# Kernel optimization log

Hardware: AMD Instinct MI355X
Metric: run time of the kernel (lower is better)

## Reference

```python
import jax, jax.numpy as jnp
import numpy as np

K = 1  # number of items to sample exactly
B, N = 512, 8192


def log1mexp(x):
    # log(1 - exp(x)) for x <= 0, numerically stable (Maechler 2012)
    return jnp.where(x > -jnp.log(2.0), jnp.log(-jnp.expm1(x)), jnp.log1p(-jnp.exp(x)))


def logaddexp_c(x1, x2):
    # custom logaddexp matching the torch module (handles -inf == -inf ties)
    delta = jnp.where(x1 == x2, 0.0, x1 - x2)
    return jnp.maximum(x1, x2) + jax.nn.softplus(-jnp.abs(delta))


def dp_table(logp, logq, kk):
    # a[b, i, c] = log Pr(exactly c-1 successes among first i items); shape [B, n+1, kk+2]
    bsz = logp.shape[0]
    state0 = jnp.full((bsz, kk + 2), -jnp.inf, logp.dtype).at[:, 1].set(0.0)
    ninf_col = jnp.full((bsz, 1), -jnp.inf, logp.dtype)

    def step(state, xs):
        lp, lq = xs  # each [B]
        grown = logaddexp_c(state[:, :-1] + lp[:, None], state[:, 1:] + lq[:, None])
        new = jnp.concatenate([ninf_col, grown], axis=1)
        return new, new

    _, rows = jax.lax.scan(step, state0, (logp.T, logq.T))  # rows: [n, B, kk+2]
    return jnp.concatenate([state0[None], rows], axis=0).transpose(1, 0, 2)


def sample_scan(a, logp, noise):
    # reverse DP sampling pass; a: [B, n+1, C], logp/noise: [B, n]
    bsz, np1, C = a.shape
    n = np1 - 1
    kcol = C - 1  # == K + 1 in table-column coordinates
    ap = a[:, :-1, :][:, ::-1].transpose(1, 0, 2)  # [n, B, C], row i-1 for i=n..1
    ac = a[:, 1:, :][:, ::-1].transpose(1, 0, 2)   # [n, B, C], row i   for i=n..1
    lp_rev = logp[:, ::-1].T                        # [n, B]
    u_rev = noise[:, ::-1].T                        # [n, B]

    def step(j, xs):
        ap_r, ac_r, lp_t, u_t = xs
        p = jnp.take_along_axis(ap_r, (j - 1)[:, None], axis=1)[:, 0]
        z = jnp.take_along_axis(ac_r, j[:, None], axis=1)[:, 0]
        p = jnp.minimum(p + lp_t - z, 0.0)  # conditional log-prob, clamp fp round-off
        q = log1mexp(p)
        X = (u_t < jax.nn.sigmoid(p - q)).astype(logp.dtype)  # Bernoulli(logits=p-q)
        j = jnp.where(X > 0, j - 1, j)
        return j, X

    j0 = jnp.full((bsz,), kcol, jnp.int32)
    _, Xs = jax.lax.scan(step, j0, (ap, ac, lp_rev, u_rev))  # Xs: [n, B]
    return Xs[::-1].T  # [B, n]


def setup_inputs() -> dict:
    key = jax.random.key(0)
    k1, k2 = jax.random.split(key)
    logits = jax.random.normal(k1, (B, N), dtype=jnp.float32)
    noise = jax.random.uniform(k2, (B, N), dtype=jnp.float32)
    return {"logits": logits, "noise": noise}


def reference(logits, noise):
    logp = jnp.minimum(jax.nn.log_sigmoid(logits), -1e-7)  # clamped log_sigmoid
    logq = log1mexp(logp)
    a = dp_table(logp, logq, K)       # [B, N+1, K+2]
    return sample_scan(a, logp, noise)  # [B, N] in {0,1}
```

## Files before the change

### kernel.cpp

```cpp
#include <hip/hip_runtime.h>
#include <math.h>

#define NB 512
#define NI 8192
#define NLOG2 0.69314718055994530942f

__device__ __forceinline__ float log1mexp_f(float x) {
    return (x > -NLOG2) ? logf(-expm1f(x)) : log1pf(-expf(x));
}

__global__ __launch_bounds__(256) void prep_kernel(const float* __restrict__ logits,
                                                   float* __restrict__ Alp,
                                                   float* __restrict__ Blq) {
    int idx = blockIdx.x * blockDim.x + threadIdx.x;
    float4 x4 = ((const float4*)logits)[idx];
    float4 lp4, lq4;
    const float* xs = &x4.x;
    float* lps = &lp4.x;
    float* lqs = &lq4.x;
#pragma unroll
    for (int j = 0; j < 4; ++j) {
        float x = xs[j];
        float lp = -(fmaxf(-x, 0.0f) + log1pf(expf(-fabsf(x))));
        lp = fminf(lp, -1e-7f);
        lps[j] = lp;
        lqs[j] = log1mexp_f(lp);
    }
    ((float4*)Alp)[idx] = lp4;
    ((float4*)Blq)[idx] = lq4;
}

#define CH 32
__device__ __forceinline__ void scan_step(float lp, float lq, float& S0, float& S1,
                                          float& x1o, float& s1o) {
    const float L2E = 1.44269504088896340736f;
    const float LN2 = 0.69314718055994530942f;
    float x1 = S0 + lp;
    float x2 = S1 + lq;
    float d  = x1 - x2;
    float m  = fmaxf(x1, x2);
    float z  = fabsf(d) * -L2E;
    float e  = __builtin_amdgcn_exp2f(z);
    float a  = 1.0f + e;
    float l  = __builtin_amdgcn_logf(a);
    S1 = fmaf(l, LN2, m);
    S0 = S0 + lq;
    x1o = x1;
    s1o = S1;
}

__global__ __launch_bounds__(64, 1) void scan_kernel(float* __restrict__ A,
                                                     float* __restrict__ B) {
    int row = blockIdx.x * blockDim.x + threadIdx.x;
    float* Ar = A + (size_t)row * NI;
    float* Br = B + (size_t)row * NI;

    float S0 = 0.0f;
    float S1 = -INFINITY;

    float lpA[CH], lqA[CH], lpB[CH], lqB[CH];
    float x1A[CH], s1A[CH], x1B[CH], s1B[CH];

#pragma unroll
    for (int j = 0; j < CH / 4; ++j) {
        *(float4*)&lpA[4 * j] = *(const float4*)&Ar[4 * j];
        *(float4*)&lqA[4 * j] = *(const float4*)&Br[4 * j];
    }

    const int NCHUNK = NI / CH;
    for (int c = 0; c < NCHUNK; c += 2) {
        const int base0 = c * CH, base1 = (c + 1) * CH, base2 = (c + 2) * CH;

#pragma unroll
        for (int j = 0; j < CH / 4; ++j) {
            *(float4*)&lpB[4 * j] = *(const float4*)&Ar[base1 + 4 * j];
            *(float4*)&lqB[4 * j] = *(const float4*)&Br[base1 + 4 * j];
        }

#pragma unroll
        for (int j = 0; j < CH; ++j)
            scan_step(lpA[j], lqA[j], S0, S1, x1A[j], s1A[j]);
#pragma unroll
        for (int j = 0; j < CH / 4; ++j) {
            *(float4*)&Ar[base0 + 4 * j] = *(float4*)&x1A[4 * j];
            *(float4*)&Br[base0 + 4 * j] = *(float4*)&s1A[4 * j];
        }

        if (c + 2 < NCHUNK) {
#pragma unroll
            for (int j = 0; j < CH / 4; ++j) {
                *(float4*)&lpA[4 * j] = *(const float4*)&Ar[base2 + 4 * j];
                *(float4*)&lqA[4 * j] = *(const float4*)&Br[base2 + 4 * j];
            }
        }

#pragma unroll
        for (int j = 0; j < CH; ++j)
            scan_step(lpB[j], lqB[j], S0, S1, x1B[j], s1B[j]);
#pragma unroll
        for (int j = 0; j < CH / 4; ++j) {
            *(float4*)&Ar[base1 + 4 * j] = *(float4*)&x1B[4 * j];
            *(float4*)&Br[base1 + 4 * j] = *(float4*)&s1B[4 * j];
        }
    }
}

__global__ __launch_bounds__(256) void decide_kernel(const float* __restrict__ A,
                                                     const float* __restrict__ S,
                                                     const float* __restrict__ noise,
                                                     float* __restrict__ out) {
    int row = blockIdx.x;
    const float4* x1r = (const float4*)(A + (size_t)row * NI);
    const float4* s1r = (const float4*)(S + (size_t)row * NI);
    const float4* ur = (const float4*)(noise + (size_t)row * NI);
    float4* outr = (float4*)(out + (size_t)row * NI);
    int tid = threadIdx.x;

    int best = -1;
#pragma unroll
    for (int k = 0; k < NI / 4 / 256; ++k) {
        int g = tid + k * 256;
        float4 x1 = x1r[g];
        float4 s1 = s1r[g];
        float4 u = ur[g];
#pragma unroll
        for (int j = 0; j < 4; ++j) {
            float p = fminf((&x1.x)[j] - (&s1.x)[j], 0.0f);
            float q = log1mexp_f(p);
            float z = p - q;
            float prob = 1.0f / (1.0f + expf(-z));
            if ((&u.x)[j] < prob) {
                int i = 4 * g + j;
                best = (i > best) ? i : best;
            }
        }
    }

#pragma unroll
    for (int off = 32; off > 0; off >>= 1) {
        int o = __shfl_down(best, off);
        best = (o > best) ? o : best;
    }
    __shared__ int lds[4];
    __shared__ int sel_s;
    int wid = tid >> 6;
    if ((tid & 63) == 0) lds[wid] = best;
    __syncthreads();
    if (tid == 0) {
        int s01 = (lds[0] > lds[1]) ? lds[0] : lds[1];
        int s23 = (lds[2] > lds[3]) ? lds[2] : lds[3];
        sel_s = (s01 > s23) ? s01 : s23;
    }
    __syncthreads();
    int sel = sel_s;

#pragma unroll
    for (int k = 0; k < NI / 4 / 256; ++k) {
        int g = tid + k * 256;
        int i0 = 4 * g;
        float4 v;
        v.x = (i0 == sel) ? 1.0f : 0.0f;
        v.y = (i0 + 1 == sel) ? 1.0f : 0.0f;
        v.z = (i0 + 2 == sel) ? 1.0f : 0.0f;
        v.w = (i0 + 3 == sel) ? 1.0f : 0.0f;
        outr[g] = v;
    }
}

extern "C" void kernel_launch(void* const* d_in, const int* in_sizes, int n_in,
                              void* d_out, int out_size, void* d_ws, size_t ws_size,
                              hipStream_t stream) {
    (void)in_sizes; (void)n_in; (void)out_size; (void)ws_size;
    const float* logits = (const float*)d_in[0];
    const float* noise = (const float*)d_in[1];
    float* out = (float*)d_out;
    float* A = (float*)d_ws;

    int total4 = NB * NI / 4;
    prep_kernel<<<total4 / 256, 256, 0, stream>>>(logits, A, out);
    scan_kernel<<<8, 64, 0, stream>>>(A, out);
    decide_kernel<<<NB, 256, 0, stream>>>(A, out, noise, out);
}
```

Before: 484.3 us.

## Fuse prep, DP scan and sampling decision into a single per-row kernel

Merges the three kernels into one. Each thread computes log-sigmoid and log1mexp inline with hardware exp2/log2 intrinsics, runs the forward recurrence, and applies the Bernoulli test on the fly while keeping the last accepted index. The one-hot output is then written per block. This removes the workspace round-trips (writing and re-reading the x1 and S1 arrays) and two kernel launches. In exchange it puts more ALU work on the serial critical path of only 8 blocks of 64 threads, uses fast approximate transcendentals that may differ slightly near decision thresholds, and simplifies sigmoid(p-q) to exp(p).

```diff
diff --git a/kernel.cpp b/kernel.cpp
--- a/kernel.cpp
+++ b/kernel.cpp
@@ -3,68 +3,57 @@
 
 #define NB 512
 #define NI 8192
-#define NLOG2 0.69314718055994530942f
+#define CH 32
 
-__device__ __forceinline__ float log1mexp_f(float x) {
-    return (x > -NLOG2) ? logf(-expm1f(x)) : log1pf(-expf(x));
-}
+__device__ __forceinline__ float fexp2(float x) { return __builtin_amdgcn_exp2f(x); }
+__device__ __forceinline__ float flog2(float x) { return __builtin_amdgcn_logf(x); }
 
-__global__ __launch_bounds__(256) void prep_kernel(const float* __restrict__ logits,
-                                                   float* __restrict__ Alp,
-                                                   float* __restrict__ Blq) {
-    int idx = blockIdx.x * blockDim.x + threadIdx.x;
-    float4 x4 = ((const float4*)logits)[idx];
-    float4 lp4, lq4;
-    const float* xs = &x4.x;
-    float* lps = &lp4.x;
-    float* lqs = &lq4.x;
-#pragma unroll
-    for (int j = 0; j < 4; ++j) {
-        float x = xs[j];
-        float lp = -(fmaxf(-x, 0.0f) + log1pf(expf(-fabsf(x))));
-        lp = fminf(lp, -1e-7f);
-        lps[j] = lp;
-        lqs[j] = log1mexp_f(lp);
-    }
-    ((float4*)Alp)[idx] = lp4;
-    ((float4*)Blq)[idx] = lq4;
-}
+#define L2E 1.44269504088896340736f
+#define LN2 0.69314718055994530942f
 
-#define CH 32
-__device__ __forceinline__ void scan_step(float lp, float lq, float& S0, float& S1,
-                                          float& x1o, float& s1o) {
-    const float L2E = 1.44269504088896340736f;
-    const float LN2 = 0.69314718055994530942f;
+__device__ __forceinline__ void step(float x, float u, int idx,
+                                     float& S0, float& S1, int& sel) {
+    float ex = fexp2(fabsf(x) * -L2E);
+    float lx = flog2(1.0f + ex);
+    float mx = fmaxf(-x, 0.0f);
+    float sp = fmaf(lx, LN2, mx);
+    float lp = fminf(-sp, -1e-7f);
+    float el = fexp2(lp * L2E);
+    float lq = flog2(1.0f - el) * LN2;
+
     float x1 = S0 + lp;
     float x2 = S1 + lq;
     float d  = x1 - x2;
     float m  = fmaxf(x1, x2);
     float z  = fabsf(d) * -L2E;
-    float e  = __builtin_amdgcn_exp2f(z);
+    float e  = fexp2(z);
     float a  = 1.0f + e;
-    float l  = __builtin_amdgcn_logf(a);
+    float l  = flog2(a);
     S1 = fmaf(l, LN2, m);
     S0 = S0 + lq;
-    x1o = x1;
-    s1o = S1;
+    float p    = fminf(x1 - S1, 0.0f);
+    float prob = fexp2(p * L2E);
+    sel = (u < prob) ? idx : sel;
 }
 
-__global__ __launch_bounds__(64, 1) void scan_kernel(float* __restrict__ A,
-                                                     float* __restrict__ B) {
-    int row = blockIdx.x * blockDim.x + threadIdx.x;
-    float* Ar = A + (size_t)row * NI;
-    float* Br = B + (size_t)row * NI;
+__global__ __launch_bounds__(64, 1) void fused_kernel(const float* __restrict__ logits,
+                                                      const float* __restrict__ noise,
+                                                      float* __restrict__ out) {
+    int lane = threadIdx.x;
+    int row  = blockIdx.x * 64 + lane;
+    const float* xr = logits + (size_t)row * NI;
+    const float* ur = noise  + (size_t)row * NI;
 
     float S0 = 0.0f;
     float S1 = -INFINITY;
+    int   sel = 0;
 
-    float lpA[CH], lqA[CH], lpB[CH], lqB[CH];
-    float x1A[CH], s1A[CH], x1B[CH], s1B[CH];
+    float xA[CH], uA[CH], xB[CH], uB[CH];
 
 #pragma unroll
     for (int j = 0; j < CH / 4; ++j) {
-        *(float4*)&lpA[4 * j] = *(const float4*)&Ar[4 * j];
-        *(float4*)&lqA[4 * j] = *(const float4*)&Br[4 * j];
+        *(float4*)&xA[4 * j] = *(const float4*)&xr[4 * j];
+        *(float4*)&uA[4 * j] = *(const float4*)&ur[4 * j];
     }
 
     const int NCHUNK = NI / CH;
@@ -73,111 +62,53 @@
 
 #pragma unroll
         for (int j = 0; j < CH / 4; ++j) {
-            *(float4*)&lpB[4 * j] = *(const float4*)&Ar[base1 + 4 * j];
-            *(float4*)&lqB[4 * j] = *(const float4*)&Br[base1 + 4 * j];
+            *(float4*)&xB[4 * j] = *(const float4*)&xr[base1 + 4 * j];
+            *(float4*)&uB[4 * j] = *(const float4*)&ur[base1 + 4 * j];
         }
-
 #pragma unroll
         for (int j = 0; j < CH; ++j)
-            scan_step(lpA[j], lqA[j], S0, S1, x1A[j], s1A[j]);
-#pragma unroll
-        for (int j = 0; j < CH / 4; ++j) {
-            *(float4*)&Ar[base0 + 4 * j] = *(float4*)&x1A[4 * j];
-            *(float4*)&Br[base0 + 4 * j] = *(float4*)&s1A[4 * j];
-        }
+            step(xA[j], uA[j], base0 + j, S0, S1, sel);
 
         if (c + 2 < NCHUNK) {
 #pragma unroll
             for (int j = 0; j < CH / 4; ++j) {
-                *(float4*)&lpA[4 * j] = *(const float4*)&Ar[base2 + 4 * j];
-                *(float4*)&lqA[4 * j] = *(const float4*)&Br[base2 + 4 * j];
+                *(float4*)&xA[4 * j] = *(const float4*)&xr[base2 + 4 * j];
+                *(float4*)&uA[4 * j] = *(const float4*)&ur[base2 + 4 * j];
             }
         }
-
 #pragma unroll
         for (int j = 0; j < CH; ++j)
-            scan_step(lpB[j], lqB[j], S0, S1, x1B[j], s1B[j]);
-#pragma unroll
-        for (int j = 0; j < CH / 4; ++j) {
-            *(float4*)&Ar[base1 + 4 * j] = *(float4*)&x1B[4 * j];
-            *(float4*)&Br[base1 + 4 * j] = *(float4*)&s1B[4 * j];
-        }
-    }
-}
-
-__global__ __launch_bounds__(256) void decide_kernel(const float* __restrict__ A,
-                                                     const float* __restrict__ S,
-                                                     const float* __restrict__ noise,
-                                                     float* __restrict__ out) {
-    int row = blockIdx.x;
-    const float4* x1r = (const float4*)(A + (size_t)row * NI);
-    const float4* s1r = (const float4*)(S + (size_t)row * NI);
-    const float4* ur = (const float4*)(noise + (size_t)row * NI);
-    float4* outr = (float4*)(out + (size_t)row * NI);
-    int tid = threadIdx.x;
-
-    int best = -1;
-#pragma unroll
-    for (int k = 0; k < NI / 4 / 256; ++k) {
-        int g = tid + k * 256;
-        float4 x1 = x1r[g];
-        float4 s1 = s1r[g];
-        float4 u = ur[g];
-#pragma unroll
-        for (int j = 0; j < 4; ++j) {
-            float p = fminf((&x1.x)[j] - (&s1.x)[j], 0.0f);
-            float q = log1mexp_f(p);
-            float z = p - q;
-            float prob = 1.0f / (1.0f + expf(-z));
-            if ((&u.x)[j] < prob) {
-                int i = 4 * g + j;
-                best = (i > best) ? i : best;
-            }
-        }
+            step(xB[j], uB[j], base1 + j, S0, S1, sel);
     }
 
+    __shared__ int sel_s[64];
+    sel_s[lane] = sel;
+    __syncthreads();
+    float4* outb = (float4*)(out + (size_t)blockIdx.x * 64 * NI);
+    for (int r = 0; r < 64; ++r) {
+        int s = sel_s[r];
+        float4* orow = outb + (size_t)r * (NI / 4);
 #pragma unroll
-    for (int off = 32; off > 0; off >>= 1) {
-        int o = __shfl_down(best, off);
-        best = (o > best) ? o : best;
-    }
-    __shared__ int lds[4];
-    __shared__ int sel_s;
-    int wid = tid >> 6;
-    if ((tid & 63) == 0) lds[wid] = best;
-    __syncthreads();
-    if (tid == 0) {
-        int s01 = (lds[0] > lds[1]) ? lds[0] : lds[1];
-        int s23 = (lds[2] > lds[3]) ? lds[2] : lds[3];
-        sel_s = (s01 > s23) ? s01 : s23;
-    }
-    __syncthreads();
-    int sel = sel_s;
-
-#pragma unroll
-    for (int k = 0; k < NI / 4 / 256; ++k) {
-        int g = tid + k * 256;
-        int i0 = 4 * g;
-        float4 v;
-        v.x = (i0 == sel) ? 1.0f : 0.0f;
-        v.y = (i0 + 1 == sel) ? 1.0f : 0.0f;
-        v.z = (i0 + 2 == sel) ? 1.0f : 0.0f;
-        v.w = (i0 + 3 == sel) ? 1.0f : 0.0f;
-        outr[g] = v;
+        for (int k = 0; k < NI / 4 / 64; ++k) {
+            int g = k * 64 + lane;
+            int i0 = 4 * g;
+            float4 v;
+            v.x = (i0     == s) ? 1.0f : 0.0f;
+            v.y = (i0 + 1 == s) ? 1.0f : 0.0f;
+            v.z = (i0 + 2 == s) ? 1.0f : 0.0f;
+            v.w = (i0 + 3 == s) ? 1.0f : 0.0f;
+            orow[g] = v;
+        }
     }
 }
 
 extern "C" void kernel_launch(void* const* d_in, const int* in_sizes, int n_in,
                               void* d_out, int out_size, void* d_ws, size_t ws_size,
                               hipStream_t stream) {
-    (void)in_sizes; (void)n_in; (void)out_size; (void)ws_size;
+    (void)in_sizes; (void)n_in; (void)out_size; (void)d_ws; (void)ws_size;
     const float* logits = (const float*)d_in[0];
-    const float* noise = (const float*)d_in[1];
+    const float* noise  = (const float*)d_in[1];
     float* out = (float*)d_out;
-    float* A = (float*)d_ws;
 
-    int total4 = NB * NI / 4;
-    prep_kernel<<<total4 / 256, 256, 0, stream>>>(logits, A, out);
-    scan_kernel<<<8, 64, 0, stream>>>(A, out);
-    decide_kernel<<<NB, 256, 0, stream>>>(A, out, noise, out);
+    fused_kernel<<<NB / 64, 64, 0, stream>>>(logits, noise, out);
 }
```

Result: slower. 777.4 us (+60.5%).
